# Kernel optimization log

Measured on AMD Instinct MI355X. Metric: run time of the kernel, lower is better.

The kernel has to match this reference:

```python
import jax, jax.numpy as jnp
import numpy as np

B, C, W, H = 8192, 512, 14, 4
D = C // H  # head dim = 128


def setup_inputs() -> dict:
    key = jax.random.key(0)
    ks = jax.random.split(key, 8)
    s = 1.0 / np.sqrt(C).astype(np.float32)
    return {
        "x": jax.random.normal(ks[0], (B, C, W), jnp.float32),
        "Wq": jax.random.normal(ks[1], (C, C), jnp.float32) * s,
        "bq": jax.random.normal(ks[2], (C,), jnp.float32) * 0.01,
        "Wk": jax.random.normal(ks[3], (C, C), jnp.float32) * s,
        "bk": jax.random.normal(ks[4], (C,), jnp.float32) * 0.01,
        "Wv": jax.random.normal(ks[5], (C, C), jnp.float32) * s,
        "bv": jax.random.normal(ks[6], (C,), jnp.float32) * 0.01,
        "rel_w": jax.random.normal(ks[7], (1, H, D, W), jnp.float32),
    }


def reference(x, Wq, bq, Wk, bk, Wv, bv, rel_w):
    # Conv1d(kernel_size=1) == channel-wise linear: out[b,o,w] = sum_c Wm[o,c]*x[b,c,w] + bm[o]
    def proj(Wm, bm):
        y = jnp.einsum('oc,bcw->bow', Wm, x) + bm[None, :, None]
        return y.reshape(B, H, D, W)

    q = proj(Wq, bq)  # [B,H,D,W]
    k = proj(Wk, bk)
    v = proj(Wv, bv)

    # content-content: q^T k over head dim -> [B,H,W,W]
    cc = jnp.einsum('bhdi,bhdj->bhij', q, k)
    # content-position: rel_w^T q -> [B,H,W,W] (rows = relative position, cols = query pos)
    cp = jnp.einsum('hdi,bhdj->bhij', rel_w[0], q)

    attn = jax.nn.softmax(cc + cp, axis=-1)  # softmax over last dim, as in the original

    # out = v @ attn^T : out[b,h,d,i] = sum_j v[b,h,d,j] * attn[b,h,i,j]
    out = jnp.einsum('bhdj,bhij->bhdi', v, attn)
    return out.reshape(B, C, W)
```

## Files before the change

### kernel.cpp

```cpp
#include <hip/hip_runtime.h>
#include <hip/hip_bf16.h>

typedef __bf16 bf16x8 __attribute__((ext_vector_type(8)));
typedef float f32x4 __attribute__((ext_vector_type(4)));
typedef int i32x4 __attribute__((ext_vector_type(4)));

typedef __attribute__((address_space(1))) const void GVoid;
typedef __attribute__((address_space(3))) void LVoid;

#define SX1 16.0f
#define SX1I 0.0625f
#define SX2 4000.0f
#define SW1 400.0f
#define SW1I 0.0025f
#define SW2 100000.0f
#define SR1 32.0f
#define SR1I 0.03125f
#define SR2 8000.0f
#define SC_QK 1.5625e-4f
#define SC_CP 1.953125e-3f
#define CORR 0.004f
#define QKS 4096.0f
#define QKSI 2.44140625e-4f
#define CPS 256.0f
#define CPSI 3.90625e-3f

static __device__ __forceinline__ float b2f(unsigned short u) {
    union { float f; unsigned int i; } x; x.i = ((unsigned int)u) << 16; return x.f;
}
static __device__ __forceinline__ unsigned short f2b(float f) {
    union { float f; unsigned int u; } x; x.f = f;
    unsigned int r = x.u + 0x7FFFu + ((x.u >> 16) & 1u);
    return (unsigned short)(r >> 16);
}
static __device__ __forceinline__ int q8v(float v, float s) {
    int i = __float2int_rn(v * s);
    return (i > 127) ? 127 : (i < -127 ? -127 : i);
}
static __device__ __forceinline__ short f2s(float v, float s) {
    int i = __float2int_rn(v * s);
    i = (i > 32767) ? 32767 : (i < -32767 ? -32767 : i);
    return (short)i;
}
static __device__ __forceinline__ float s2f(unsigned int pair, int hi, float sc) {
    short s = hi ? (short)(pair >> 16) : (short)(pair & 0xffffu);
    return (float)s * sc;
}

__global__ __launch_bounds__(256) void k_prep(const float* __restrict__ Wq, const float* __restrict__ Wk,
                                              const float* __restrict__ Wv, const float* __restrict__ bq,
                                              const float* __restrict__ bk, const float* __restrict__ bv,
                                              const float* __restrict__ relw, char* __restrict__ Wi8,
                                              float* __restrict__ biasA) {
    int o = blockIdx.x;
    int tid = threadIdx.x;
    if (o < 1024) {
        const float* src = (o < 512) ? (Wq + (long)o * 512) : (Wk + (long)(o - 512) * 512);
        char* row = Wi8 + (long)o * 1024;
        for (int c = tid; c < 512; c += 256) {
            float w = src[c];
            int wh = q8v(w, SW1);
            float res = w - (float)wh * SW1I;
            int wl = q8v(res, SW2);
            row[c] = (char)wh;
            row[512 + c] = (char)wl;
        }
    } else if (o < 1536) {
        const float* src = Wv + (long)(o - 1024) * 512;
        char* row = Wi8 + (long)(1152 + (o - 1024)) * 1024;
        for (int c = tid; c < 512; c += 256) {
            float w = src[c];
            int wh = q8v(w, SW1);
            float res = w - (float)wh * SW1I;
            int wl = q8v(res, SW2);
            row[c] = (char)wh;
            row[512 + c] = (char)wl;
        }
    } else if (o < 1592) {
        int t = o - 1536, h = t / 14, i = t - h * 14;
        char* row = Wi8 + (long)(1024 + t) * 1024;
#pragma unroll
        for (int cc = 0; cc < 2; ++cc) {
            int c = tid + cc * 256;
            float acc = 0.f;
            for (int d = 0; d < 128; ++d)
                acc += relw[h * 1792 + d * 14 + i] * Wq[(long)(h * 128 + d) * 512 + c];
            int rh = q8v(acc, SR1);
            float res = acc - (float)rh * SR1I;
            int rl = q8v(res, SR2);
            row[c] = (char)rh;
            row[512 + c] = (char)rl;
        }
        if (tid == 0) {
            float acc = 0.f;
            for (int d = 0; d < 128; ++d) acc += relw[h * 1792 + d * 14 + i] * bq[h * 128 + d];
            biasA[1024 + t] = acc;
        }
    } else {
        for (int i = tid; i < 1664; i += 256) {
            if (i >= 1024 && i < 1080) continue;
            biasA[i] = (i < 512) ? bq[i] : (i < 1024) ? bk[i - 512] : (i < 1152) ? 0.f : bv[i - 1152];
        }
        int* z = (int*)(Wi8 + (long)1080 * 1024);
        for (int idx = tid; idx < 72 * 256; idx += 256) z[idx] = 0;
    }
}

__global__ __launch_bounds__(256) void k_transpose(const float* __restrict__ x,
                                                   char* __restrict__ Ai8, int b0) {
    __shared__ float xl[512 * 15];
    const float* xb = x + (long)(b0 + blockIdx.x) * 7168;
    const float4* xb4 = (const float4*)xb;
    int tid = threadIdx.x;
#pragma unroll
    for (int it = 0; it < 7; ++it) {
        int f = tid + it * 256;
        float4 v = xb4[f];
        float vals[4] = {v.x, v.y, v.z, v.w};
        int e = f * 4;
#pragma unroll
        for (int j = 0; j < 4; ++j) {
            int ee = e + j;
            int c = (ee * 9363) >> 17;
            int w = ee - c * 14;
            xl[c * 15 + w] = vals[j];
        }
    }
    __syncthreads();
    char* irow = Ai8 + (long)blockIdx.x * 14336;
#pragma unroll
    for (int it = 0; it < 7; ++it) {
        int p = tid + it * 256;
        int w = p >> 7, c0 = (p & 127) * 4;
        unsigned int hp = 0, lp = 0;
#pragma unroll
        for (int j = 0; j < 4; ++j) {
            float v = xl[(c0 + j) * 15 + w];
            int xh = q8v(v, SX1);
            float res = v - (float)xh * SX1I;
            int xlo = q8v(res, SX2);
            hp |= ((unsigned int)(xh & 255)) << (8 * j);
            lp |= ((unsigned int)(xlo & 255)) << (8 * j);
        }
        *(unsigned int*)(irow + (long)w * 1024 + c0) = hp;
        *(unsigned int*)(irow + (long)w * 1024 + 512 + c0) = lp;
    }
}

__global__ __launch_bounds__(256, 2) void k_gemmA(const char* __restrict__ Ai8,
                                                  const char* __restrict__ Wi8,
                                                  const float* __restrict__ biasA,
                                                  short* __restrict__ qkI,
                                                  unsigned short* __restrict__ vb, int Mtiles) {
    __shared__ __align__(16) char Ls[2][4][128 * 64];
    int nwg = Mtiles * 13;
    int p = blockIdx.x;
    int xcd = p & 7, o8 = p >> 3;
    int q8_ = nwg >> 3, r8 = nwg & 7;
    int t = (xcd < r8 ? xcd * (q8_ + 1) : r8 * (q8_ + 1) + (xcd - r8) * q8_) + o8;
    int mt = t / 13, nt = t - mt * 13;
    long m0 = (long)mt * 128;
    int n0 = nt * 128;
    bool isv = (nt >= 9);
    int tid = threadIdx.x, lane = tid & 63, wv = tid >> 6;
    int wr = wv >> 1, wc = wv & 1;

    i32x4 accM[4][4], accC[4][4];
#pragma unroll
    for (int i = 0; i < 4; ++i)
#pragma unroll
        for (int j = 0; j < 4; ++j) { accM[i][j] = (i32x4){0, 0, 0, 0}; accC[i][j] = (i32x4){0, 0, 0, 0}; }

#define STAGE(KT, BUF)                                                                           \
    {                                                                                            \
        int kof = (KT) * 64;                                                                     \
        _Pragma("unroll") for (int i = 0; i < 2; ++i) {                                          \
            int row = i * 64 + (tid >> 2);                                                       \
            int gu = (((tid & 3) + (row >> 1)) & 3) << 4;                                        \
            long ao = ((m0 + row) << 10) + kof + gu;                                             \
            long bo = ((long)(n0 + row) << 10) + kof + gu;                                       \
            int dof = i * 4096 + tid * 16;                                                       \
            __builtin_amdgcn_global_load_lds((GVoid*)(Ai8 + ao), (LVoid*)(&Ls[BUF][0][0] + dof), 16, 0, 0); \
            __builtin_amdgcn_global_load_lds((GVoid*)(Ai8 + ao + 512), (LVoid*)(&Ls[BUF][1][0] + dof), 16, 0, 0); \
            __builtin_amdgcn_global_load_lds((GVoid*)(Wi8 + bo), (LVoid*)(&Ls[BUF][2][0] + dof), 16, 0, 0); \
            __builtin_amdgcn_global_load_lds((GVoid*)(Wi8 + bo + 512), (LVoid*)(&Ls[BUF][3][0] + dof), 16, 0, 0); \
        }                                                                                        \
    }

    STAGE(0, 0);
    int cur = 0;
    for (int kt = 0; kt < 8; ++kt) {
        if (kt < 7) {
            if (cur == 0) STAGE(kt + 1, 1) else STAGE(kt + 1, 0);
            asm volatile("s_waitcnt vmcnt(8)" ::: "memory");
        } else {
            asm volatile("s_waitcnt vmcnt(0)" ::: "memory");
        }
        __builtin_amdgcn_s_barrier();
        __builtin_amdgcn_sched_barrier(0);

        const char* Ah = &Ls[cur][0][0];
        const char* Al = &Ls[cur][1][0];
        const char* Bh = &Ls[cur][2][0];
        const char* Bl = &Ls[cur][3][0];
        int U = lane >> 4;
        i32x4 ah[4], al[4], bh[4], bl[4];
#pragma unroll
        for (int mf = 0; mf < 4; ++mf) {
            int row = wr * 64 + mf * 16 + (lane & 15);
            ah[mf] = *(const i32x4*)(Ah + row * 64 + (((U - (row >> 1)) & 3) << 4));
        }
#pragma unroll
        for (int nf = 0; nf < 4; ++nf) {
            int row = wc * 64 + nf * 16 + (lane & 15);
            bh[nf] = *(const i32x4*)(Bh + row * 64 + (((U - (row >> 1)) & 3) << 4));
        }
#pragma unroll
        for (int mf = 0; mf < 4; ++mf) {
            int row = wr * 64 + mf * 16 + (lane & 15);
            al[mf] = *(const i32x4*)(Al + row * 64 + (((U - (row >> 1)) & 3) << 4));
        }
#pragma unroll
        for (int nf = 0; nf < 4; ++nf) {
            int row = wc * 64 + nf * 16 + (lane & 15);
            bl[nf] = *(const i32x4*)(Bl + row * 64 + (((U - (row >> 1)) & 3) << 4));
        }
        __builtin_amdgcn_s_setprio(1);
#pragma unroll
        for (int mf = 0; mf < 4; ++mf)
#pragma unroll
            for (int nf = 0; nf < 4; ++nf)
                accM[mf][nf] = __builtin_amdgcn_mfma_i32_16x16x64_i8(ah[mf], bh[nf], accM[mf][nf], 0, 0, 0);
#pragma unroll
        for (int mf = 0; mf < 4; ++mf)
#pragma unroll
            for (int nf = 0; nf < 4; ++nf) {
                accC[mf][nf] = __builtin_amdgcn_mfma_i32_16x16x64_i8(ah[mf], bl[nf], accC[mf][nf], 0, 0, 0);
                accC[mf][nf] = __builtin_amdgcn_mfma_i32_16x16x64_i8(al[mf], bh[nf], accC[mf][nf], 0, 0, 0);
            }
        __builtin_amdgcn_s_setprio(0);
        __builtin_amdgcn_sched_barrier(0);
        __builtin_amdgcn_s_barrier();
        cur ^= 1;
    }
#undef STAGE

    unsigned short* eb = (unsigned short*)&Ls[0][0][0];
#pragma unroll
    for (int nf = 0; nf < 4; ++nf) {
        int ncol = wc * 64 + nf * 16 + (lane & 15);
        int n = n0 + ncol;
        float scale = (n < 1024) ? SC_QK : (n < 1152 ? SC_CP : SC_QK);
        float qsc = (n < 1024) ? QKS : CPS;
        float bb = biasA[n];
#pragma unroll
        for (int mf = 0; mf < 4; ++mf) {
            int rl0 = wr * 64 + mf * 16 + ((lane >> 4) << 2);
#pragma unroll
            for (int r = 0; r < 4; ++r) {
                float val = ((float)accM[mf][nf][r] + CORR * (float)accC[mf][nf][r]) * scale + bb;
                unsigned short sv = isv ? f2b(val) : (unsigned short)f2s(val, qsc);
                int row = rl0 + r;
                eb[row * 128 + ((((ncol >> 3) ^ (row & 7)) << 3) | (ncol & 7))] = sv;
            }
        }
    }
    __syncthreads();
    {
        int row = tid >> 1, half = tid & 1;
        long rb = isv ? ((m0 + row) * 1024 + (long)(n0 - 1152) * 2)
                      : ((m0 + row) * 2304 + (long)n0 * 2);
        char* dst = (isv ? (char*)vb : (char*)qkI) + rb + half * 128;
        const char* src = (const char*)eb + row * 256;
#pragma unroll
        for (int j = 0; j < 8; ++j) {
            int u = half * 8 + j;
            int up = u ^ (row & 7);
            *(uint4*)(dst + j * 16) = *(const uint4*)(src + up * 16);
        }
    }
}

__global__ __launch_bounds__(512) void k_attn(const short* __restrict__ qkI,
                                              const unsigned short* __restrict__ vb,
                                              float* __restrict__ out, int b0) {
    __shared__ float qs[14 * 512];
    __shared__ float ks[14 * 512];
    __shared__ float cps[56 * 16];
    __shared__ float sl[56 * 16];
    __shared__ unsigned short vs[14 * 512];
    int tid = threadIdx.x;
    long mb = (long)blockIdx.x * 14;
    const uint4* qk16 = (const uint4*)qkI;
#pragma unroll
    for (int it = 0; it < 4; ++it) {
        int idx = tid + it * 512;
        if (idx < 1792) {
            int w = idx >> 7, c8 = idx & 127;
            uint4 raw = qk16[(mb + w) * 144 + c8];
            float4 f0 = make_float4(s2f(raw.x, 0, QKSI), s2f(raw.x, 1, QKSI),
                                    s2f(raw.y, 0, QKSI), s2f(raw.y, 1, QKSI));
            float4 f1 = make_float4(s2f(raw.z, 0, QKSI), s2f(raw.z, 1, QKSI),
                                    s2f(raw.w, 0, QKSI), s2f(raw.w, 1, QKSI));
            float* base = (c8 < 64) ? qs : ks;
            int uu0 = (c8 & 63) * 2;
            *(float4*)&base[w * 512 + ((uu0 ^ (w & 7)) << 2)] = f0;
            *(float4*)&base[w * 512 + (((uu0 + 1) ^ (w & 7)) << 2)] = f1;
        }
    }
#pragma unroll
    for (int it = 0; it < 2; ++it) {
        int idx = tid + it * 512;
        if (idx < 784) {
            int w = idx / 56, tt = idx - w * 56;
            cps[tt * 16 + w] = (float)qkI[(mb + w) * 1152 + 1024 + tt] * CPSI;
        }
    }
#pragma unroll
    for (int it = 0; it < 2; ++it) {
        int idx = tid + it * 512;
        if (idx < 896) {
            int w = idx >> 6, uu = idx & 63;
            *(uint4*)&vs[w * 512 + uu * 8] = *(const uint4*)&vb[(mb + w) * 512 + uu * 8];
        }
    }
    __syncthreads();
    if (tid < 196) {
        int h = tid / 49, r = tid - h * 49;
        int i0 = (r / 7) * 2, j0 = (r - (r / 7) * 7) * 2;
        float a00 = 0.f, a01 = 0.f, a10 = 0.f, a11 = 0.f;
#pragma unroll
        for (int d4 = 0; d4 < 32; ++d4) {
            int uu = h * 32 + d4;
            float4 qa = *(const float4*)&qs[i0 * 512 + ((uu ^ (i0 & 7)) << 2)];
            float4 qb = *(const float4*)&qs[(i0 + 1) * 512 + ((uu ^ ((i0 + 1) & 7)) << 2)];
            float4 ka = *(const float4*)&ks[j0 * 512 + ((uu ^ (j0 & 7)) << 2)];
            float4 kb = *(const float4*)&ks[(j0 + 1) * 512 + ((uu ^ ((j0 + 1) & 7)) << 2)];
            a00 += qa.x * ka.x + qa.y * ka.y + qa.z * ka.z + qa.w * ka.w;
            a01 += qa.x * kb.x + qa.y * kb.y + qa.z * kb.z + qa.w * kb.w;
            a10 += qb.x * ka.x + qb.y * ka.y + qb.z * ka.z + qb.w * ka.w;
            a11 += qb.x * kb.x + qb.y * kb.y + qb.z * kb.z + qb.w * kb.w;
        }
        int base = (h * 14 + i0) * 16 + j0;
        sl[base] = a00 + cps[base];
        sl[base + 1] = a01 + cps[base + 1];
        sl[base + 16] = a10 + cps[base + 16];
        sl[base + 17] = a11 + cps[base + 17];
    }
    __syncthreads();
    if (tid < 56) {
        float* row = &sl[tid * 16];
        float m = row[0];
#pragma unroll
        for (int j = 1; j < 14; ++j) m = fmaxf(m, row[j]);
        float ex[14]; float sum = 0.f;
#pragma unroll
        for (int j = 0; j < 14; ++j) { ex[j] = __expf(row[j] - m); sum += ex[j]; }
        float inv = 1.f / sum;
#pragma unroll
        for (int j = 0; j < 14; ++j) row[j] = ex[j] * inv;
    }
    __syncthreads();
    int c = tid, h = c >> 7;
    float vr[14];
#pragma unroll
    for (int j = 0; j < 14; ++j) vr[j] = b2f(vs[j * 512 + c]);
    float* orow = out + (((long)(b0 + blockIdx.x) * 512 + c) * 14);
    float ob[14];
#pragma unroll
    for (int i = 0; i < 14; ++i) {
        const float* ar = &sl[(h * 14 + i) * 16];
        float a = 0.f;
#pragma unroll
        for (int j = 0; j < 14; ++j) a += vr[j] * ar[j];
        ob[i] = a;
    }
#pragma unroll
    for (int t2 = 0; t2 < 7; ++t2)
        *(float2*)(orow + t2 * 2) = make_float2(ob[2 * t2], ob[2 * t2 + 1]);
}

extern "C" void kernel_launch(void* const* d_in, const int* in_sizes, int n_in,
                              void* d_out, int out_size, void* d_ws, size_t ws_size,
                              hipStream_t stream) {
    const float* x    = (const float*)d_in[0];
    const float* Wq   = (const float*)d_in[1];
    const float* bq   = (const float*)d_in[2];
    const float* Wk   = (const float*)d_in[3];
    const float* bk   = (const float*)d_in[4];
    const float* Wv   = (const float*)d_in[5];
    const float* bv   = (const float*)d_in[6];
    const float* relw = (const float*)d_in[7];
    float* out = (float*)d_out;
    char* ws = (char*)d_ws;

    char*  Wi8   = ws;
    float* biasA = (float*)(ws + 1703936);
    const long WS_DATA = 1712128;

    long avail = (long)ws_size - WS_DATA;
    long nbmax = avail / 60928;
    long NBc = (nbmax / 128) * 128;
    if (NBc > 8192) NBc = 8192;
    if (NBc < 128) NBc = 128;

    char*           Ai8 = ws + WS_DATA;
    short*          qkI = (short*)(Ai8 + NBc * 14336);
    unsigned short* vbw = (unsigned short*)(qkI + NBc * 16128);

    k_prep<<<1593, 256, 0, stream>>>(Wq, Wk, Wv, bq, bk, bv, relw, Wi8, biasA);

    for (int b0 = 0; b0 < 8192; b0 += (int)NBc) {
        int nb = 8192 - b0; if (nb > NBc) nb = (int)NBc;
        int Mtiles = (nb * 14) / 128;
        k_transpose<<<nb, 256, 0, stream>>>(x, Ai8, b0);
        k_gemmA<<<Mtiles * 13, 256, 0, stream>>>(Ai8, Wi8, biasA, qkI, vbw, Mtiles);
        k_attn<<<nb, 512, 0, stream>>>(qkI, vbw, out, b0);
    }
}
```

Before: 668.5 us.

## Skip low-part MFMA for V tiles, read cp/V directly, cap chunk size

For tiles producing V, the GEMM no longer loads the low-part B fragments or issues the A_hi*B_lo correction MFMA, which cuts MFMA work and LDS reads on those tiles but gives V slightly lower precision. The attention kernel drops the cps and vs shared-memory staging: cp values are read directly from global memory as packed pairs, and V is read straight from global per thread. This saves LDS space and staging passes, at the cost of more scattered global loads. The batch chunk size is also capped at 2048, so more launches are issued, but the intermediates are more likely to stay in cache between the GEMM and attention kernels.

Measured after the change: 665.5 us. No clear change (-0.4%).

```diff
diff --git a/kernel.cpp b/kernel.cpp
--- a/kernel.cpp
+++ b/kernel.cpp
@@ -220,10 +220,12 @@
             int row = wr * 64 + mf * 16 + (lane & 15);
             al[mf] = *(const i32x4*)(Al + row * 64 + (((U - (row >> 1)) & 3) << 4));
         }
-#pragma unroll
-        for (int nf = 0; nf < 4; ++nf) {
-            int row = wc * 64 + nf * 16 + (lane & 15);
-            bl[nf] = *(const i32x4*)(Bl + row * 64 + (((U - (row >> 1)) & 3) << 4));
+        if (!isv) {
+#pragma unroll
+            for (int nf = 0; nf < 4; ++nf) {
+                int row = wc * 64 + nf * 16 + (lane & 15);
+                bl[nf] = *(const i32x4*)(Bl + row * 64 + (((U - (row >> 1)) & 3) << 4));
+            }
         }
         __builtin_amdgcn_s_setprio(1);
 #pragma unroll
@@ -235,8 +237,9 @@
         for (int mf = 0; mf < 4; ++mf)
 #pragma unroll
             for (int nf = 0; nf < 4; ++nf) {
-                accC[mf][nf] = __builtin_amdgcn_mfma_i32_16x16x64_i8(ah[mf], bl[nf], accC[mf][nf], 0, 0, 0);
                 accC[mf][nf] = __builtin_amdgcn_mfma_i32_16x16x64_i8(al[mf], bh[nf], accC[mf][nf], 0, 0, 0);
+                if (!isv)
+                    accC[mf][nf] = __builtin_amdgcn_mfma_i32_16x16x64_i8(ah[mf], bl[nf], accC[mf][nf], 0, 0, 0);
             }
         __builtin_amdgcn_s_setprio(0);
         __builtin_amdgcn_sched_barrier(0);
@@ -286,9 +289,7 @@
                                               float* __restrict__ out, int b0) {
     __shared__ float qs[14 * 512];
     __shared__ float ks[14 * 512];
-    __shared__ float cps[56 * 16];
     __shared__ float sl[56 * 16];
-    __shared__ unsigned short vs[14 * 512];
     int tid = threadIdx.x;
     long mb = (long)blockIdx.x * 14;
     const uint4* qk16 = (const uint4*)qkI;
@@ -308,22 +309,6 @@
             *(float4*)&base[w * 512 + (((uu0 + 1) ^ (w & 7)) << 2)] = f1;
         }
     }
-#pragma unroll
-    for (int it = 0; it < 2; ++it) {
-        int idx = tid + it * 512;
-        if (idx < 784) {
-            int w = idx / 56, tt = idx - w * 56;
-            cps[tt * 16 + w] = (float)qkI[(mb + w) * 1152 + 1024 + tt] * CPSI;
-        }
-    }
-#pragma unroll
-    for (int it = 0; it < 2; ++it) {
-        int idx = tid + it * 512;
-        if (idx < 896) {
-            int w = idx >> 6, uu = idx & 63;
-            *(uint4*)&vs[w * 512 + uu * 8] = *(const uint4*)&vb[(mb + w) * 512 + uu * 8];
-        }
-    }
     __syncthreads();
     if (tid < 196) {
         int h = tid / 49, r = tid - h * 49;
@@ -341,11 +326,13 @@
             a10 += qb.x * ka.x + qb.y * ka.y + qb.z * ka.z + qb.w * ka.w;
             a11 += qb.x * kb.x + qb.y * kb.y + qb.z * kb.z + qb.w * kb.w;
         }
+        unsigned int cpa = *(const unsigned int*)&qkI[(mb + j0) * 1152 + 1024 + h * 14 + i0];
+        unsigned int cpb = *(const unsigned int*)&qkI[(mb + j0 + 1) * 1152 + 1024 + h * 14 + i0];
         int base = (h * 14 + i0) * 16 + j0;
-        sl[base] = a00 + cps[base];
-        sl[base + 1] = a01 + cps[base + 1];
-        sl[base + 16] = a10 + cps[base + 16];
-        sl[base + 17] = a11 + cps[base + 17];
+        sl[base]      = a00 + s2f(cpa, 0, CPSI);
+        sl[base + 16] = a10 + s2f(cpa, 1, CPSI);
+        sl[base + 1]  = a01 + s2f(cpb, 0, CPSI);
+        sl[base + 17] = a11 + s2f(cpb, 1, CPSI);
     }
     __syncthreads();
     if (tid < 56) {
@@ -364,7 +351,7 @@
     int c = tid, h = c >> 7;
     float vr[14];
 #pragma unroll
-    for (int j = 0; j < 14; ++j) vr[j] = b2f(vs[j * 512 + c]);
+    for (int j = 0; j < 14; ++j) vr[j] = b2f(vb[(mb + j) * 512 + c]);
     float* orow = out + (((long)(b0 + blockIdx.x) * 512 + c) * 14);
     float ob[14];
 #pragma unroll
@@ -401,7 +388,7 @@
     long avail = (long)ws_size - WS_DATA;
     long nbmax = avail / 60928;
     long NBc = (nbmax / 128) * 128;
-    if (NBc > 8192) NBc = 8192;
+    if (NBc > 2048) NBc = 2048;
     if (NBc < 128) NBc = 128;
 
     char*           Ai8 = ws + WS_DATA;
```
